# Kernel tuning notes

Hardware: AMD Instinct MI355X
Metric: run time of the kernel (lower is better)

The kernel has to match this reference:

```python
import jax, jax.numpy as jnp
import numpy as np

HEADS = 20
HEAD_DIM = 64
NUM_TOKENS = 4


def _split_heads(x, B):
    # (B, S, H*D) -> (B, H, S, D)
    return x.reshape(B, -1, HEADS, HEAD_DIM).transpose(0, 2, 1, 3)


def setup_inputs() -> dict:
    key = jax.random.key(0)
    ks = jax.random.split(key, 10)
    B, HW, hid, cad, Ltxt = 2, 4096, 1280, 2048, 77
    w = lambda k, shp: (jax.random.normal(k, shp, jnp.float32) * 0.02)
    return {
        "hidden_states": jax.random.normal(ks[0], (B, HW, hid), jnp.float32),
        "encoder_hidden_states": jax.random.normal(ks[1], (B, Ltxt + NUM_TOKENS, cad), jnp.float32),
        "indices_to_alter": jax.random.randint(ks[2], (B,), 0, Ltxt, jnp.int32),
        "Wq": w(ks[3], (hid, hid)),
        "Wk": w(ks[4], (cad, hid)),
        "Wv": w(ks[5], (cad, hid)),
        "Wk_nest": w(ks[6], (cad, hid)),
        "Wv_nest": w(ks[7], (cad, hid)),
        "Wout": w(ks[8], (hid, hid)),
        "b_out": jnp.zeros((hid,), jnp.float32),
    }


def reference(hidden_states, encoder_hidden_states, indices_to_alter,
              Wq, Wk, Wv, Wk_nest, Wv_nest, Wout, b_out):
    B, HW, _ = hidden_states.shape
    end = encoder_hidden_states.shape[1] - NUM_TOKENS
    txt = encoder_hidden_states[:, :end]   # (B, Ltxt, cad)
    img = encoder_hidden_states[:, end:]   # (B, num_tokens, cad)

    q = _split_heads(hidden_states @ Wq, B)   # (B, H, HW, D)
    k = _split_heads(txt @ Wk, B)             # (B, H, Lt, D)
    v = _split_heads(txt @ Wv, B)             # (B, H, Lt, D)
    kn = _split_heads(img @ Wk_nest, B)       # (B, H, T, D)
    vn = _split_heads(img @ Wv_nest, B)       # (B, H, T, D)

    sc = 1.0 / jnp.sqrt(jnp.float32(HEAD_DIM))

    # nested attention: per-spatial-position identity value V* (SDPA over image tokens)
    wn = jax.nn.softmax(jnp.einsum('bhqd,bhkd->bhqk', q, kn) * sc, axis=-1)
    value_id = jnp.einsum('bhqk,bhkd->bhqd', wn, vn)          # (B, H, HW, D)

    # main cross attention over text tokens
    w = jax.nn.softmax(jnp.einsum('bhqd,bhkd->bhqk', q, k) * sc, axis=-1)  # (B,H,HW,Lt)
    base = jnp.einsum('bhqk,bhkd->bhqd', w, v)                # (B, H, HW, D)

    # V_mixed[b,h,i] differs from value only at text slot s_b, where it equals value_id[b,h,i].
    # sum_k w[...,k] * V_mixed[...,k,:] == w @ v + w[...,s]*(value_id - v[:, :, s])
    s = indices_to_alter
    w_s = jnp.take_along_axis(w, s[:, None, None, None], axis=3)   # (B, H, HW, 1)
    v_s = jnp.take_along_axis(v, s[:, None, None, None], axis=2)   # (B, H, 1, D)
    out = base + w_s * (value_id - v_s)                             # (B, H, HW, D)

    out = out.transpose(0, 2, 1, 3).reshape(B, HW, HEADS * HEAD_DIM)
    return out @ Wout + b_out
```

## Files before the change

### kernel.cpp

```cpp
#include <hip/hip_runtime.h>
#include <hip/hip_bf16.h>


typedef unsigned short ushort_t;
typedef __attribute__((ext_vector_type(8))) short short8;
typedef __attribute__((ext_vector_type(4))) float f32x4;

#define B_   2
#define HW_  4096
#define HID_ 1280
#define CAD_ 2048
#define LTXT 77
#define NTOK 4
#define NH_  20
#define HD_  64

__device__ __forceinline__ ushort_t f2bf(float f) {
    __hip_bfloat16 h = __float2bfloat16(f);
    return *reinterpret_cast<ushort_t*>(&h);
}

__device__ __forceinline__ void gld_lds16(const void* g, void* l) {
    __builtin_amdgcn_global_load_lds(
        (const __attribute__((address_space(1))) unsigned int*)g,
        (__attribute__((address_space(3))) unsigned int*)l,
        16, 0, 0);
}

__global__ __launch_bounds__(256) void prep(
    const float* __restrict__ hs, const float* __restrict__ enc,
    const float* __restrict__ s0, const float* __restrict__ s1,
    const float* __restrict__ s2, const float* __restrict__ s3,
    const float* __restrict__ s4, const float* __restrict__ s5,
    ushort_t* __restrict__ hsb, ushort_t* __restrict__ encb,
    ushort_t* __restrict__ d0, ushort_t* __restrict__ d1,
    ushort_t* __restrict__ d2, ushort_t* __restrict__ d3,
    ushort_t* __restrict__ d4, ushort_t* __restrict__ d5)
{
    const int y = blockIdx.y, t = threadIdx.x;
    if (y <= 1) {
        const float* src = y ? enc : hs;
        ushort_t* dst = y ? encb : hsb;
        int n4 = y ? (B_ * (LTXT + NTOK) * CAD_) / 4 : (B_ * HW_ * HID_) / 4;
        int step = gridDim.x * 256;
        for (int i = blockIdx.x * 256 + t; i < n4; i += step) {
            float4 v = *(const float4*)(src + (size_t)i * 4);
            ushort_t o[4] = { f2bf(v.x), f2bf(v.y), f2bf(v.z), f2bf(v.w) };
            *(uint2*)(dst + (size_t)i * 4) = *(uint2*)o;
        }
        return;
    }
    int z = y - 2;
    const float* S; ushort_t* D; int K_;
    switch (z) {
        case 0: S = s0; D = d0; K_ = 1280; break;
        case 1: S = s1; D = d1; K_ = 2048; break;
        case 2: S = s2; D = d2; K_ = 2048; break;
        case 3: S = s3; D = d3; K_ = 2048; break;
        case 4: S = s4; D = d4; K_ = 2048; break;
        default: S = s5; D = d5; K_ = 1280; break;
    }
    int tr = blockIdx.x / 40, tc = blockIdx.x % 40;
    if (tr >= K_ / 32) return;
    __shared__ ushort_t tl[32][33];
    int c = t & 31, r0 = t >> 5;
#pragma unroll
    for (int i = 0; i < 4; i++) {
        int r = r0 + i * 8;
        tl[r][c] = f2bf(S[(size_t)(tr * 32 + r) * 1280 + tc * 32 + c]);
    }
    __syncthreads();
#pragma unroll
    for (int i = 0; i < 4; i++) {
        int r = r0 + i * 8;
        D[(size_t)(tc * 32 + r) * K_ + tr * 32 + c] = tl[c][r];
    }
}

template <bool F32OUT>
__device__ __forceinline__ void gemm_body(
    const ushort_t* __restrict__ A, const ushort_t* __restrict__ Bt,
    void* __restrict__ Cout, const float* __restrict__ biasf,
    int M, int K, int lda, int row0, int col0)
{
    __shared__ ushort_t lsA[128 * 32];
    __shared__ ushort_t lsB[128 * 32];
    const int t = threadIdx.x;
    const int w = t >> 6, l = t & 63;
    const int mb = (w >> 1) * 64, nb = (w & 1) * 64;
    const int lrow = l & 15, lk = (l >> 4) * 8;
    f32x4 acc[4][4] = {};
    for (int k0 = 0; k0 < K; k0 += 32) {
        __syncthreads();
#pragma unroll
        for (int p = 0; p < 2; p++) {
            int lin = p * 256 + t;
            int r = lin >> 2, cc = (lin & 3) * 8;
            int ra = row0 + r; if (ra > M - 1) ra = M - 1;
            gld_lds16(A + (size_t)ra * lda + k0 + cc, &lsA[lin * 8]);
            int rb = col0 + r;
            gld_lds16(Bt + (size_t)rb * K + k0 + cc, &lsB[lin * 8]);
        }
        __syncthreads();
        short8 af[4], bfr[4];
#pragma unroll
        for (int mt = 0; mt < 4; mt++)
            af[mt] = *(const short8*)&lsA[(mb + mt * 16 + lrow) * 32 + lk];
#pragma unroll
        for (int nt = 0; nt < 4; nt++)
            bfr[nt] = *(const short8*)&lsB[(nb + nt * 16 + lrow) * 32 + lk];
#pragma unroll
        for (int mt = 0; mt < 4; mt++)
#pragma unroll
            for (int nt = 0; nt < 4; nt++)
                acc[mt][nt] = __builtin_amdgcn_mfma_f32_16x16x32_bf16(
                    af[mt], bfr[nt], acc[mt][nt], 0, 0, 0);
    }
    const int quad = l >> 4, cl = l & 15;
#pragma unroll
    for (int nt = 0; nt < 4; nt++) {
        int col = col0 + nb + nt * 16 + cl;
        float bv = biasf ? biasf[col] : 0.f;
#pragma unroll
        for (int mt = 0; mt < 4; mt++)
#pragma unroll
            for (int r = 0; r < 4; r++) {
                int row = row0 + mb + mt * 16 + quad * 4 + r;
                if (row < M) {
                    if (F32OUT)
                        ((float*)Cout)[(size_t)row * 1280 + col] = acc[mt][nt][r] + bv;
                    else
                        ((ushort_t*)Cout)[(size_t)row * 1280 + col] = f2bf(acc[mt][nt][r] + bv);
                }
            }
    }
}

__global__ __launch_bounds__(256, 3) void gemm_q_kv(
    const ushort_t* __restrict__ hsb, const ushort_t* __restrict__ encb,
    const ushort_t* __restrict__ WqT,
    const ushort_t* __restrict__ WkT, const ushort_t* __restrict__ WvT,
    const ushort_t* __restrict__ WknT, const ushort_t* __restrict__ WvnT,
    ushort_t* __restrict__ qb, ushort_t* __restrict__ kb, ushort_t* __restrict__ vb,
    ushort_t* __restrict__ knb, ushort_t* __restrict__ vnb)
{
    int x = blockIdx.x, col0 = blockIdx.y * 128;
    if (x < 64) {
        gemm_body<false>(hsb, WqT, qb, nullptr, B_ * HW_, HID_, HID_, x * 128, col0);
        return;
    }
    int z = x - 64, kind = z & 1;
    const ushort_t* A; const ushort_t* Bt; ushort_t* C; int M;
    if (z < 4) {
        int bb = z >> 1;
        M = LTXT;
        A = encb + (size_t)bb * (LTXT + NTOK) * CAD_;
        Bt = kind ? WvT : WkT;
        C = (kind ? vb : kb) + (size_t)bb * LTXT * HID_;
    } else {
        int bb = (z - 4) >> 1;
        M = NTOK;
        A = encb + ((size_t)bb * (LTXT + NTOK) + LTXT) * CAD_;
        Bt = kind ? WvnT : WknT;
        C = (kind ? vnb : knb) + (size_t)bb * NTOK * HID_;
    }
    gemm_body<false>(A, Bt, C, nullptr, M, CAD_, CAD_, 0, col0);
}

__global__ __launch_bounds__(256, 3) void gemm_bt_f32(
    const ushort_t* __restrict__ A, const ushort_t* __restrict__ Bt,
    float* __restrict__ C, const float* __restrict__ biasf, int M, int K, int lda)
{
    gemm_body<true>(A, Bt, C, biasf, M, K, lda, blockIdx.x * 128, blockIdx.y * 128);
}

__global__ __launch_bounds__(256, 3) void attn_kernel(
    const ushort_t* __restrict__ qb, const ushort_t* __restrict__ kbf,
    const ushort_t* __restrict__ vbf, const ushort_t* __restrict__ knb,
    const ushort_t* __restrict__ vnb, const int* __restrict__ sidx,
    ushort_t* __restrict__ ob)
{
    const int qt = blockIdx.x, h = blockIdx.y, b = blockIdx.z;
    const int t = threadIdx.x, w = t >> 6, l = t & 63;
    const int s_idx = sidx[b];
    __shared__ ushort_t Kl[96 * 72];
    __shared__ ushort_t VT[64 * 104];
    __shared__ ushort_t QP[128 * 104];

    for (int id = t; id < 96 * 8; id += 256) {
        int key = id >> 3, c = (id & 7) * 8;
        uint4 v;
        if (key < LTXT)
            v = *(const uint4*)&kbf[((size_t)(b * LTXT + key)) * HID_ + h * HD_ + c];
        else if (key >= 80 && key < 80 + NTOK)
            v = *(const uint4*)&knb[((size_t)(b * NTOK + key - 80)) * HID_ + h * HD_ + c];
        else
            v = make_uint4(0u, 0u, 0u, 0u);
        *(uint4*)&Kl[key * 72 + c] = v;
    }
    for (int id = t; id < 64 * 96; id += 256) {
        int d = id / 96, key = id - d * 96;
        ushort_t val = 0;
        if (key < LTXT)
            val = vbf[((size_t)(b * LTXT + key)) * HID_ + h * HD_ + d];
        else if (key >= 80 && key < 80 + NTOK)
            val = vnb[((size_t)(b * NTOK + key - 80)) * HID_ + h * HD_ + d];
        VT[d * 104 + key] = val;
    }
    const int q0 = qt * 128;
    for (int id = t; id < 128 * 8; id += 256) {
        int r = id >> 3, c = (id & 7) * 8;
        uint4 v = *(const uint4*)&qb[((size_t)(b * HW_ + q0 + r)) * HID_ + h * HD_ + c];
        *(uint4*)&QP[r * 72 + c] = v;
    }
    __syncthreads();

    const int mbw = w * 32, lrow = l & 15, lk = (l >> 4) * 8;
    const int quad = l >> 4, cl = l & 15;

    f32x4 S[2][6] = {};
#pragma unroll
    for (int ks = 0; ks < 2; ks++) {
        short8 af0 = *(const short8*)&QP[(mbw + lrow) * 72 + ks * 32 + lk];
        short8 af1 = *(const short8*)&QP[(mbw + 16 + lrow) * 72 + ks * 32 + lk];
#pragma unroll
        for (int nt = 0; nt < 6; nt++) {
            short8 bf = *(const short8*)&Kl[(nt * 16 + lrow) * 72 + ks * 32 + lk];
            S[0][nt] = __builtin_amdgcn_mfma_f32_16x16x32_bf16(af0, bf, S[0][nt], 0, 0, 0);
            S[1][nt] = __builtin_amdgcn_mfma_f32_16x16x32_bf16(af1, bf, S[1][nt], 0, 0, 0);
        }
    }
    __syncthreads();

    const float sc = 0.125f;
#pragma unroll
    for (int mt = 0; mt < 2; mt++) {
#pragma unroll
        for (int r = 0; r < 4; r++) {
            float v[6];
#pragma unroll
            for (int nt = 0; nt < 6; nt++) v[nt] = S[mt][nt][r] * sc;
            float m = -1e30f;
#pragma unroll
            for (int nt = 0; nt < 5; nt++) {
                int c = nt * 16 + cl;
                if (c < LTXT) m = fmaxf(m, v[nt]);
            }
#pragma unroll
            for (int off = 1; off < 16; off <<= 1) m = fmaxf(m, __shfl_xor(m, off));
            float e[5], lsum = 0.f, wsn = 0.f;
#pragma unroll
            for (int nt = 0; nt < 5; nt++) {
                int c = nt * 16 + cl;
                float ev = (c < LTXT) ? __expf(v[nt] - m) : 0.f;
                e[nt] = ev; lsum += ev;
                if (c == s_idx) wsn += ev;
            }
#pragma unroll
            for (int off = 1; off < 16; off <<= 1) {
                lsum += __shfl_xor(lsum, off);
                wsn  += __shfl_xor(wsn, off);
            }
            float inv = 1.f / lsum;
            float ws = wsn * inv;
            bool nv = (cl < 4);
            float m5 = nv ? v[5] : -1e30f;
#pragma unroll
            for (int off = 1; off < 16; off <<= 1) m5 = fmaxf(m5, __shfl_xor(m5, off));
            float e5 = nv ? __expf(v[5] - m5) : 0.f;
            float l5 = e5;
#pragma unroll
            for (int off = 1; off < 16; off <<= 1) l5 += __shfl_xor(l5, off);
            float p5 = ws * e5 / l5;
            int row = mbw + mt * 16 + quad * 4 + r;
#pragma unroll
            for (int nt = 0; nt < 5; nt++) {
                int c = nt * 16 + cl;
                float p = (c < LTXT && c != s_idx) ? e[nt] * inv : 0.f;
                QP[row * 104 + c] = f2bf(p);
            }
            QP[row * 104 + 80 + cl] = f2bf(p5);
        }
    }
    __syncthreads();

    f32x4 O[2][4] = {};
#pragma unroll
    for (int ks = 0; ks < 3; ks++) {
        short8 af0 = *(const short8*)&QP[(mbw + lrow) * 104 + ks * 32 + lk];
        short8 af1 = *(const short8*)&QP[(mbw + 16 + lrow) * 104 + ks * 32 + lk];
#pragma unroll
        for (int nt = 0; nt < 4; nt++) {
            short8 bf = *(const short8*)&VT[(nt * 16 + lrow) * 104 + ks * 32 + lk];
            O[0][nt] = __builtin_amdgcn_mfma_f32_16x16x32_bf16(af0, bf, O[0][nt], 0, 0, 0);
            O[1][nt] = __builtin_amdgcn_mfma_f32_16x16x32_bf16(af1, bf, O[1][nt], 0, 0, 0);
        }
    }
#pragma unroll
    for (int mt = 0; mt < 2; mt++)
#pragma unroll
        for (int nt = 0; nt < 4; nt++)
#pragma unroll
            for (int r = 0; r < 4; r++) {
                int row = mbw + mt * 16 + quad * 4 + r;
                int d = nt * 16 + cl;
                ob[((size_t)(b * HW_ + q0 + row)) * HID_ + h * HD_ + d] = f2bf(O[mt][nt][r]);
            }
}

extern "C" void kernel_launch(void* const* d_in, const int* in_sizes, int n_in,
                              void* d_out, int out_size, void* d_ws, size_t ws_size,
                              hipStream_t stream) {
    const float* hs   = (const float*)d_in[0];
    const float* enc  = (const float*)d_in[1];
    const int*   idx  = (const int*)d_in[2];
    const float* Wq   = (const float*)d_in[3];
    const float* Wk   = (const float*)d_in[4];
    const float* Wv   = (const float*)d_in[5];
    const float* Wkn  = (const float*)d_in[6];
    const float* Wvn  = (const float*)d_in[7];
    const float* Wout = (const float*)d_in[8];
    const float* bout = (const float*)d_in[9];
    float* out = (float*)d_out;

    ushort_t* ws = (ushort_t*)d_ws;
    size_t o = 0;
    ushort_t* WqT   = ws + o; o += (size_t)1280 * 1280;
    ushort_t* WkT   = ws + o; o += (size_t)1280 * 2048;
    ushort_t* WvT   = ws + o; o += (size_t)1280 * 2048;
    ushort_t* WknT  = ws + o; o += (size_t)1280 * 2048;
    ushort_t* WvnT  = ws + o; o += (size_t)1280 * 2048;
    ushort_t* WoutT = ws + o; o += (size_t)1280 * 1280;
    ushort_t* hsb   = ws + o; o += (size_t)B_ * HW_ * HID_;
    ushort_t* encb  = ws + o; o += (size_t)B_ * (LTXT + NTOK) * CAD_;
    ushort_t* qbuf  = ws + o; o += (size_t)B_ * HW_ * HID_;
    ushort_t* kbuf  = ws + o; o += (size_t)B_ * LTXT * HID_;
    ushort_t* vbuf  = ws + o; o += (size_t)B_ * LTXT * HID_;
    ushort_t* knbuf = ws + o; o += (size_t)B_ * NTOK * HID_;
    ushort_t* vnbuf = ws + o; o += (size_t)B_ * NTOK * HID_;
    ushort_t* attnb = hsb;

    prep<<<dim3(2560, 8), 256, 0, stream>>>(hs, enc, Wq, Wk, Wv, Wkn, Wvn, Wout,
                                            hsb, encb,
                                            WqT, WkT, WvT, WknT, WvnT, WoutT);
    gemm_q_kv<<<dim3(72, 10), 256, 0, stream>>>(hsb, encb, WqT, WkT, WvT, WknT, WvnT,
                                                qbuf, kbuf, vbuf, knbuf, vnbuf);
    attn_kernel<<<dim3(HW_ / 128, NH_, B_), 256, 0, stream>>>(qbuf, kbuf, vbuf,
                                                              knbuf, vnbuf, idx, attnb);
    gemm_bt_f32<<<dim3(64, 10), 256, 0, stream>>>(attnb, WoutT, out, bout,
                                                  B_ * HW_, HID_, HID_);
}
```

Measured before the change: 289.7 us.

## Double-buffer GEMM LDS tiles, raise occupancy bound, vectorize V transpose load

The shared GEMM body now double-buffers its A/B LDS tiles, issuing the async global-to-LDS loads for the next K-slice before the MFMAs on the current one, with a single barrier per iteration. Launch bounds on the two GEMM kernels rise from 3 to 4 blocks per CU. The attention kernel's V-transpose staging now loads 16-byte vectors per key and scatters them into LDS instead of doing scalar global loads. Together these target global-load latency and the cost of the scalar V gather, at the price of twice the GEMM LDS footprint, which may limit how many blocks actually fit per CU.

```diff
diff --git a/kernel.cpp b/kernel.cpp
--- a/kernel.cpp
+++ b/kernel.cpp
@@ -83,39 +83,52 @@
     void* __restrict__ Cout, const float* __restrict__ biasf,
     int M, int K, int lda, int row0, int col0)
 {
-    __shared__ ushort_t lsA[128 * 32];
-    __shared__ ushort_t lsB[128 * 32];
+    __shared__ ushort_t lsA[2][128 * 32];
+    __shared__ ushort_t lsB[2][128 * 32];
     const int t = threadIdx.x;
     const int w = t >> 6, l = t & 63;
     const int mb = (w >> 1) * 64, nb = (w & 1) * 64;
     const int lrow = l & 15, lk = (l >> 4) * 8;
+
+    const int r0s = t >> 2, cs = (t & 3) * 8;
+    int ra0 = row0 + r0s;       if (ra0 > M - 1) ra0 = M - 1;
+    int ra1 = row0 + r0s + 64;  if (ra1 > M - 1) ra1 = M - 1;
+    const ushort_t* gA0 = A + (size_t)ra0 * lda + cs;
+    const ushort_t* gA1 = A + (size_t)ra1 * lda + cs;
+    const ushort_t* gB0 = Bt + (size_t)(col0 + r0s) * K + cs;
+    const ushort_t* gB1 = Bt + (size_t)(col0 + r0s + 64) * K + cs;
+
+#define STAGE_(bf, k0) do { \
+        gld_lds16(gA0 + (k0), &lsA[bf][(size_t)t * 8]); \
+        gld_lds16(gA1 + (k0), &lsA[bf][(size_t)(256 + t) * 8]); \
+        gld_lds16(gB0 + (k0), &lsB[bf][(size_t)t * 8]); \
+        gld_lds16(gB1 + (k0), &lsB[bf][(size_t)(256 + t) * 8]); \
+    } while (0)
+
     f32x4 acc[4][4] = {};
+    STAGE_(0, 0);
+    __syncthreads();
+    int cur = 0;
     for (int k0 = 0; k0 < K; k0 += 32) {
-        __syncthreads();
-#pragma unroll
-        for (int p = 0; p < 2; p++) {
-            int lin = p * 256 + t;
-            int r = lin >> 2, cc = (lin & 3) * 8;
-            int ra = row0 + r; if (ra > M - 1) ra = M - 1;
-            gld_lds16(A + (size_t)ra * lda + k0 + cc, &lsA[lin * 8]);
-            int rb = col0 + r;
-            gld_lds16(Bt + (size_t)rb * K + k0 + cc, &lsB[lin * 8]);
-        }
-        __syncthreads();
+        if (k0 + 32 < K) STAGE_(cur ^ 1, k0 + 32);
         short8 af[4], bfr[4];
 #pragma unroll
         for (int mt = 0; mt < 4; mt++)
-            af[mt] = *(const short8*)&lsA[(mb + mt * 16 + lrow) * 32 + lk];
+            af[mt] = *(const short8*)&lsA[cur][(mb + mt * 16 + lrow) * 32 + lk];
 #pragma unroll
         for (int nt = 0; nt < 4; nt++)
-            bfr[nt] = *(const short8*)&lsB[(nb + nt * 16 + lrow) * 32 + lk];
+            bfr[nt] = *(const short8*)&lsB[cur][(nb + nt * 16 + lrow) * 32 + lk];
 #pragma unroll
         for (int mt = 0; mt < 4; mt++)
 #pragma unroll
             for (int nt = 0; nt < 4; nt++)
                 acc[mt][nt] = __builtin_amdgcn_mfma_f32_16x16x32_bf16(
                     af[mt], bfr[nt], acc[mt][nt], 0, 0, 0);
-    }
+        __syncthreads();
+        cur ^= 1;
+    }
+#undef STAGE_
+
     const int quad = l >> 4, cl = l & 15;
 #pragma unroll
     for (int nt = 0; nt < 4; nt++) {
@@ -136,7 +149,7 @@
     }
 }
 
-__global__ __launch_bounds__(256, 3) void gemm_q_kv(
+__global__ __launch_bounds__(256, 4) void gemm_q_kv(
     const ushort_t* __restrict__ hsb, const ushort_t* __restrict__ encb,
     const ushort_t* __restrict__ WqT,
     const ushort_t* __restrict__ WkT, const ushort_t* __restrict__ WvT,
@@ -167,7 +180,7 @@
     gemm_body<false>(A, Bt, C, nullptr, M, CAD_, CAD_, 0, col0);
 }
 
-__global__ __launch_bounds__(256, 3) void gemm_bt_f32(
+__global__ __launch_bounds__(256, 4) void gemm_bt_f32(
     const ushort_t* __restrict__ A, const ushort_t* __restrict__ Bt,
     float* __restrict__ C, const float* __restrict__ biasf, int M, int K, int lda)
 {
@@ -198,14 +211,20 @@
             v = make_uint4(0u, 0u, 0u, 0u);
         *(uint4*)&Kl[key * 72 + c] = v;
     }
-    for (int id = t; id < 64 * 96; id += 256) {
-        int d = id / 96, key = id - d * 96;
-        ushort_t val = 0;
-        if (key < LTXT)
-            val = vbf[((size_t)(b * LTXT + key)) * HID_ + h * HD_ + d];
-        else if (key >= 80 && key < 80 + NTOK)
-            val = vnb[((size_t)(b * NTOK + key - 80)) * HID_ + h * HD_ + d];
-        VT[d * 104 + key] = val;
+    for (int c8 = (t >> 7); c8 < 8; c8 += 2) {
+        int key = t & 127;
+        if (key < 96) {
+            uint4 v = make_uint4(0u, 0u, 0u, 0u);
+            if (key < LTXT)
+                v = *(const uint4*)&vbf[((size_t)(b * LTXT + key)) * HID_ + h * HD_ + c8 * 8];
+            else if (key >= 80 && key < 80 + NTOK)
+                v = *(const uint4*)&vnb[((size_t)(b * NTOK + key - 80)) * HID_ + h * HD_ + c8 * 8];
+            ushort_t tmp[8];
+            *(uint4*)tmp = v;
+#pragma unroll
+            for (int j = 0; j < 8; j++)
+                VT[(c8 * 8 + j) * 104 + key] = tmp[j];
+        }
     }
     const int q0 = qt * 128;
     for (int id = t; id < 128 * 8; id += 256) {
```

Result: faster. 276.9 us (-4.4%).
